# Kernel optimization log

Measured on AMD Instinct MI355X. Metric: run time of the kernel, lower is better.

Reference implementation:

```python
import jax, jax.numpy as jnp
import numpy as np

L, B, T, C, H, V = 12, 4, 1024, 768, 12, 50257
D = C // H
SCALE = 1.0 / float(np.sqrt(D))
EPS = 1e-5


def layernorm(x, g, b):
    m = jnp.mean(x, axis=-1, keepdims=True)
    v = jnp.var(x, axis=-1, keepdims=True)
    return (x - m) / jnp.sqrt(v + EPS) * g + b


def setup_inputs() -> dict:
    key = jax.random.key(0)
    ks = jax.random.split(key, 12)
    w = lambda k, shape: jax.random.normal(k, shape, jnp.float32) * 0.02
    return {
        "idx": jax.random.randint(ks[0], (B, T), 0, V),
        "tok_emb": w(ks[1], (V, C)),
        "pos_emb": w(ks[2], (1, T, C)),
        # per-layer stacked params (leading dim L); Linear stored [in, out]
        "wq": w(ks[3], (L, C, C)), "bq": jnp.zeros((L, C)),
        "wk": w(ks[4], (L, C, C)), "bk": jnp.zeros((L, C)),
        "wv": w(ks[5], (L, C, C)), "bv": jnp.zeros((L, C)),
        "wo": w(ks[6], (L, C, C)), "bo": jnp.zeros((L, C)),
        "ln1_g": jnp.ones((L, C)), "ln1_b": jnp.zeros((L, C)),
        "ln2_g": jnp.ones((L, C)), "ln2_b": jnp.zeros((L, C)),
        "w1": w(ks[7], (L, C, 4 * C)), "b1": jnp.zeros((L, 4 * C)),
        "w2": w(ks[8], (L, 4 * C, C)), "b2": jnp.zeros((L, C)),
        "lnf_g": jnp.ones((C,)), "lnf_b": jnp.zeros((C,)),
        "head_w": w(ks[9], (C, V)),
    }


def gpt_forward(idx, tok_emb, pos_emb, wq, bq, wk, bk, wv, bv, wo, bo,
                ln1_g, ln1_b, ln2_g, ln2_b, w1, b1, w2, b2,
                lnf_g, lnf_b, head_w):
    t = idx.shape[1]
    x = tok_emb[idx] + pos_emb[:, :t, :]                     # [B,T,C]
    mask = jnp.tril(jnp.ones((t, t), dtype=bool))            # causal

    def block(x, p):
        (pwq, pbq, pwk, pbk, pwv, pbv, pwo, pbo,
         g1, be1, g2, be2, pw1, pb1, pw2, pb2) = p
        h = layernorm(x, g1, be1)
        q = (h @ pwq + pbq).reshape(B, t, H, D)
        k = (h @ pwk + pbk).reshape(B, t, H, D)
        v = (h @ pwv + pbv).reshape(B, t, H, D)
        att = jnp.einsum('bthd,bshd->bhts', q, k) * SCALE    # [B,H,T,T]
        att = jnp.where(mask, att, -jnp.inf)
        att = jax.nn.softmax(att, axis=-1)
        y = jnp.einsum('bhts,bshd->bthd', att, v).reshape(B, t, C)
        x = x + y @ pwo + pbo
        h = layernorm(x, g2, be2)
        x = x + jax.nn.gelu(h @ pw1 + pb1, approximate=False) @ pw2 + pb2
        return x, None

    x, _ = jax.lax.scan(block, x, (wq, bq, wk, bk, wv, bv, wo, bo,
                                   ln1_g, ln1_b, ln2_g, ln2_b,
                                   w1, b1, w2, b2))
    x = layernorm(x, lnf_g, lnf_b)
    return x @ head_w                                        # logits [B,T,V]


def reference(idx, tok_emb, pos_emb, wq, bq, wk, bk, wv, bv, wo, bo,
              ln1_g, ln1_b, ln2_g, ln2_b, w1, b1, w2, b2,
              lnf_g, lnf_b, head_w):
    return gpt_forward(idx, tok_emb, pos_emb, wq, bq, wk, bk, wv, bv, wo, bo,
                       ln1_g, ln1_b, ln2_g, ln2_b, w1, b1, w2, b2,
                       lnf_g, lnf_b, head_w)
```

## Files before the change

### kernel.cpp

```cpp
#include <hip/hip_runtime.h>
#include <hip/hip_bf16.h>
#include <math.h>

#define L_ 12
#define B_ 4
#define T_ 1024
#define C_ 768
#define H_ 12
#define D_ 64
#define V_ 50257
#define M_ 4096
#define QKVN 2304
#define FF_ 3072
#define VPAD_ 51200

typedef __hip_bfloat16 bf16;
typedef __attribute__((ext_vector_type(4))) float f32x4;
typedef __attribute__((ext_vector_type(4))) short short4v;
typedef __attribute__((ext_vector_type(8))) short short8;
typedef __attribute__((ext_vector_type(8))) __bf16 bf16x8;

typedef __attribute__((address_space(1))) void gvoid;
typedef __attribute__((address_space(3))) void svoid;

__device__ __forceinline__ f32x4 mfma_bf16(short8 a, short8 b, f32x4 c) {
  return __builtin_amdgcn_mfma_f32_16x16x32_bf16(
      __builtin_bit_cast(bf16x8, a), __builtin_bit_cast(bf16x8, b), c, 0, 0, 0);
}

__device__ __forceinline__ void gload_lds16(const void* g, void* l) {
  __builtin_amdgcn_global_load_lds((gvoid*)(void*)g, (svoid*)l, 16, 0, 0);
}

__device__ __forceinline__ short f2bf(float x) {
  return __builtin_bit_cast(short, __float2bfloat16(x));
}

__global__ __launch_bounds__(256) void embed_kernel(const int* __restrict__ idx,
    const float* __restrict__ tok, const float* __restrict__ pos, float* __restrict__ x)
{
  const int row = blockIdx.x;
  const int t = row & (T_ - 1);
  const int id = idx[row];
  const float* te = tok + (size_t)id * C_;
  const float* pe = pos + (size_t)t * C_;
  float* xr = x + (size_t)row * C_;
  const int tid = threadIdx.x;
  xr[tid]       = te[tid]       + pe[tid];
  xr[tid + 256] = te[tid + 256] + pe[tid + 256];
  xr[tid + 512] = te[tid + 512] + pe[tid + 512];
}

__global__ __launch_bounds__(256) void ln_kernel(const float* __restrict__ x,
    const float* __restrict__ g, const float* __restrict__ be, bf16* __restrict__ out)
{
  const int w = threadIdx.x >> 6, l = threadIdx.x & 63;
  const int row = blockIdx.x * 4 + w;
  const float* xr = x + (size_t)row * C_;
  f32x4 v[3];
  float s = 0.0f, ss = 0.0f;
#pragma unroll
  for (int p = 0; p < 3; p++) {
    v[p] = *(const f32x4*)&xr[p * 256 + l * 4];
#pragma unroll
    for (int e = 0; e < 4; e++) { s += v[p][e]; ss += v[p][e] * v[p][e]; }
  }
#pragma unroll
  for (int o = 32; o >= 1; o >>= 1) { s += __shfl_xor(s, o, 64); ss += __shfl_xor(ss, o, 64); }
  const float mean = s * (1.0f / C_);
  const float rstd = rsqrtf(ss * (1.0f / C_) - mean * mean + 1e-5f);
  bf16* orow = out + (size_t)row * C_;
#pragma unroll
  for (int p = 0; p < 3; p++) {
    const f32x4 gg = *(const f32x4*)&g[p * 256 + l * 4];
    const f32x4 bb = *(const f32x4*)&be[p * 256 + l * 4];
    short4v o4;
#pragma unroll
    for (int e = 0; e < 4; e++) o4[e] = f2bf((v[p][e] - mean) * rstd * gg[e] + bb[e]);
    *(short4v*)&orow[p * 256 + l * 4] = o4;
  }
}

__global__ __launch_bounds__(256) void convt_kernel(const float* __restrict__ in,
    bf16* __restrict__ out, int K, int N, long in_ls, long out_ls, int row_off)
{
  __shared__ float tile[64][65];
  in  += (size_t)blockIdx.z * in_ls;
  out += (size_t)blockIdx.z * out_ls;
  const int k0 = blockIdx.x * 64, n0 = blockIdx.y * 64;
  const int tid = threadIdx.x;
#pragma unroll
  for (int ph = 0; ph < 4; ph++) {
    const int lk = ph * 16 + (tid >> 4);
    const int ln = (tid & 15) * 4;
    const int gn = n0 + ln;
    const float* src = &in[(size_t)(k0 + lk) * N + gn];
    f32x4 vv;
    if (gn + 4 <= N) {
      vv = *(const f32x4*)src;
    } else {
#pragma unroll
      for (int e = 0; e < 4; e++) vv[e] = (gn + e < N) ? src[e] : 0.0f;
    }
    *(f32x4*)&tile[lk][ln] = vv;
  }
  __syncthreads();
#pragma unroll
  for (int ph = 0; ph < 2; ph++) {
    const int lon = ph * 32 + (tid >> 3);
    const int lok0 = (tid & 7) * 8;
    short8 o;
#pragma unroll
    for (int e = 0; e < 8; e++) o[e] = f2bf(tile[lok0 + e][lon]);
    *(short8*)&out[(size_t)(row_off + n0 + lon) * K + k0 + lok0] = o;
  }
}

__global__ __launch_bounds__(256) void packb_kernel(const float* __restrict__ bq,
    const float* __restrict__ bk, const float* __restrict__ bv, float* __restrict__ out)
{
  const int i = blockIdx.x * 256 + threadIdx.x;
  const int ly = i / QKVN, c = i % QKVN;
  float v;
  if (c < C_)            v = bq[ly * C_ + c];
  else if (c < 2 * C_)   v = bk[ly * C_ + c - C_];
  else                   v = bv[ly * C_ + c - 2 * C_];
  out[i] = v;
}

template<bool BIAS, bool GELU, bool RESID, bool BF16OUT, bool VT>
__global__ __launch_bounds__(256) void gemm_bt(
    const short* __restrict__ A, const short* __restrict__ Bt,
    const float* __restrict__ bias, const float* resid,
    void* out, short* __restrict__ vt, int M, int N, int K)
{
  __shared__ short As[128 * 64];
  __shared__ short Bs[128 * 64];
  const int tid = threadIdx.x;
  const int w = tid >> 6, l = tid & 63;
  const int l15 = l & 15, l4 = l >> 4;
  const int wr = w >> 1, wc = w & 1;
  const int nwg = gridDim.x * gridDim.y;
  const int id = blockIdx.y * gridDim.x + blockIdx.x;
  const int chunk = nwg >> 3;
  const int swz = (id & 7) * chunk + (id >> 3);
  const long m0 = (long)(swz % gridDim.x) * 128;
  const long n0 = (long)(swz / gridDim.x) * 128;

  f32x4 acc[4][4] = {};
  const int lrow8 = l >> 3;
  const int lc = l & 7;

  for (int kt = 0; kt < K; kt += 64) {
#pragma unroll
    for (int j = 0; j < 8; j++) {
      const int c = w * 8 + j;
      const int isA = (c < 16);
      const int cc = isA ? c : (c - 16);
      const int row = cc * 8 + lrow8;
      const int colsw = ((lc ^ (row & 7)) << 3);
      const short* gp = (isA ? A + (size_t)(m0 + row) * K : Bt + (size_t)(n0 + row) * K) + kt + colsw;
      short* sp = (isA ? As : Bs) + row * 64 + (lc << 3);
      gload_lds16(gp, sp);
    }
    __syncthreads();
#pragma unroll
    for (int ks = 0; ks < 2; ks++) {
      short8 af[4], bfr[4];
#pragma unroll
      for (int i = 0; i < 4; i++) {
        int row = wr * 64 + i * 16 + l15;
        int cs = (ks * 32 + l4 * 8) ^ ((row & 7) << 3);
        af[i] = *(const short8*)&As[row * 64 + cs];
      }
#pragma unroll
      for (int jn = 0; jn < 4; jn++) {
        int row = wc * 64 + jn * 16 + l15;
        int cs = (ks * 32 + l4 * 8) ^ ((row & 7) << 3);
        bfr[jn] = *(const short8*)&Bs[row * 64 + cs];
      }
#pragma unroll
      for (int i = 0; i < 4; i++)
#pragma unroll
        for (int jn = 0; jn < 4; jn++)
          acc[i][jn] = mfma_bf16(af[i], bfr[jn], acc[i][jn]);
    }
    __syncthreads();
  }

#pragma unroll
  for (int i = 0; i < 4; i++) {
    const long rbase = m0 + wr * 64 + i * 16 + l4 * 4;
#pragma unroll
    for (int jn = 0; jn < 4; jn++) {
      const long col = n0 + wc * 64 + jn * 16 + l15;
      const float bv = BIAS ? bias[col] : 0.0f;
      if (VT && col >= 2 * C_) {
        const int hd = (int)col - 2 * C_;
        const int b = (int)(rbase >> 10);
        const int t0 = (int)(rbase & 1023);
        short4v o4;
#pragma unroll
        for (int r = 0; r < 4; r++) o4[r] = f2bf(acc[i][jn][r] + bv);
        *(short4v*)&vt[((size_t)(b * H_) * D_ + hd) * T_ + t0] = o4;
      } else {
#pragma unroll
        for (int r = 0; r < 4; r++) {
          float v = acc[i][jn][r] + bv;
          if (GELU) v = 0.5f * v * (1.0f + erff(v * 0.70710678118654752f));
          const size_t o = (size_t)(rbase + r) * (size_t)N + col;
          if (RESID)        ((float*)out)[o] = resid[o] + v;
          else if (BF16OUT) ((bf16*)out)[o] = __float2bfloat16(v);
          else              ((float*)out)[o] = v;
        }
      }
    }
  }
}

template<bool BIAS, bool GELU, bool RESID, bool BF16OUT>
__global__ __launch_bounds__(256) void gemm64(
    const short* __restrict__ A, const short* __restrict__ Bt,
    const float* __restrict__ bias, const float* resid,
    void* out, int M, int N, int K)
{
  __shared__ short As[64 * 64];
  __shared__ short Bs[128 * 64];
  const int tid = threadIdx.x;
  const int w = tid >> 6, l = tid & 63;
  const int l15 = l & 15, l4 = l >> 4;
  const int wm = w >> 1, wn = w & 1;
  const int nwg = gridDim.x * gridDim.y;
  const int id = blockIdx.y * gridDim.x + blockIdx.x;
  const int chunk = nwg >> 3;
  const int swz = (id & 7) * chunk + (id >> 3);
  const long m0 = (long)(swz % gridDim.x) * 64;
  const long n0 = (long)(swz / gridDim.x) * 128;
  const int rr = tid >> 3, g = tid & 7;

  f32x4 acc[2][4] = {};

  for (int kt = 0; kt < K; kt += 64) {
#pragma unroll
    for (int p = 0; p < 2; p++) {
      const int row = p * 32 + rr;
      const int cg = ((g ^ (row & 7)) << 3);
      gload_lds16(A + (size_t)(m0 + row) * K + kt + cg, &As[row * 64 + g * 8]);
    }
#pragma unroll
    for (int p = 0; p < 4; p++) {
      const int row = p * 32 + rr;
      const int cg = ((g ^ (row & 7)) << 3);
      gload_lds16(Bt + (size_t)(n0 + row) * K + kt + cg, &Bs[row * 64 + g * 8]);
    }
    __syncthreads();
#pragma unroll
    for (int ks = 0; ks < 2; ks++) {
      short8 af[2], bfr[4];
#pragma unroll
      for (int i = 0; i < 2; i++) {
        int row = wm * 32 + i * 16 + l15;
        int cs = (ks * 32 + l4 * 8) ^ ((row & 7) << 3);
        af[i] = *(const short8*)&As[row * 64 + cs];
      }
#pragma unroll
      for (int j = 0; j < 4; j++) {
        int row = wn * 64 + j * 16 + l15;
        int cs = (ks * 32 + l4 * 8) ^ ((row & 7) << 3);
        bfr[j] = *(const short8*)&Bs[row * 64 + cs];
      }
#pragma unroll
      for (int i = 0; i < 2; i++)
#pragma unroll
        for (int j = 0; j < 4; j++)
          acc[i][j] = mfma_bf16(af[i], bfr[j], acc[i][j]);
    }
    __syncthreads();
  }

#pragma unroll
  for (int i = 0; i < 2; i++) {
    const long rbase = m0 + wm * 32 + i * 16 + l4 * 4;
#pragma unroll
    for (int j = 0; j < 4; j++) {
      const long col = n0 + wn * 64 + j * 16 + l15;
      const float bv = BIAS ? bias[col] : 0.0f;
#pragma unroll
      for (int r = 0; r < 4; r++) {
        float v = acc[i][j][r] + bv;
        if (GELU) v = 0.5f * v * (1.0f + erff(v * 0.70710678118654752f));
        const size_t o = (size_t)(rbase + r) * (size_t)N + col;
        if (RESID)        ((float*)out)[o] = resid[o] + v;
        else if (BF16OUT) ((bf16*)out)[o] = __float2bfloat16(v);
        else              ((float*)out)[o] = v;
      }
    }
  }
}

__global__ __launch_bounds__(512, 1) void gemm256(
    const short* __restrict__ A, const short* __restrict__ Bt,
    float* __restrict__ out, int N, int K)
{
  __shared__ short As[2][256 * 64];
  __shared__ short Bs[2][256 * 64];
  const int tid = threadIdx.x;
  const int l = tid & 63, l15 = l & 15, l4 = l >> 4;
  const int wv = tid >> 6, wm = wv >> 2, wn = wv & 3;
  const int bid = blockIdx.x;
  const int x = bid & 7, r = bid >> 3;
  const int mt = (x & 1) * 8 + (r & 7);
  const int nt = (x >> 1) * 50 + (r >> 3);
  const long m0 = (long)mt * 256;
  const long n0 = (long)nt * 256;
  const int nkt = K >> 6;
  const int rr = tid >> 3, g = tid & 7;

  f32x4 acc[8][4] = {};

  auto stA = [&](int s, int kt, int off) {
#pragma unroll
    for (int p = 0; p < 2; p++) {
      const int row = p * 128 + off + rr;
      gload_lds16(A + (size_t)(m0 + row) * K + (kt << 6) + ((g ^ (row & 7)) << 3),
                  &As[s][row * 64 + g * 8]);
    }
  };
  auto stB = [&](int s, int kt, int off) {
#pragma unroll
    for (int p = 0; p < 2; p++) {
      const int row = p * 128 + ((rr >> 5) << 6) + (rr & 31) + off;
      gload_lds16(Bt + (size_t)(n0 + row) * K + (kt << 6) + ((g ^ (row & 7)) << 3),
                  &Bs[s][row * 64 + g * 8]);
    }
  };
  auto rdA = [&](int s, int mf, int ks) {
    const int row = wm * 128 + mf * 16 + l15;
    const int cs = (ks * 32 + l4 * 8) ^ ((row & 7) << 3);
    return *(const short8*)&As[s][row * 64 + cs];
  };
  auto rdB = [&](int s, int nf, int ks) {
    const int row = wn * 64 + nf * 16 + l15;
    const int cs = (ks * 32 + l4 * 8) ^ ((row & 7) << 3);
    return *(const short8*)&Bs[s][row * 64 + cs];
  };

  stA(0, 0, 0); stB(0, 0, 0); stA(0, 0, 64); stB(0, 0, 32);

  int q = 0;
  for (int kt = 0; kt < nkt; ++kt, q ^= 1) {
    const int ktn = (kt + 1 < nkt) ? kt + 1 : kt;
    short8 a0[2][4], a1[2][4], b0[2][2], b1[2][2];

    stA(q ^ 1, ktn, 0);
    asm volatile("s_waitcnt vmcnt(6)" ::: "memory");
    __builtin_amdgcn_s_barrier();
#pragma unroll
    for (int ks = 0; ks < 2; ks++) {
#pragma unroll
      for (int f = 0; f < 4; f++) a0[ks][f] = rdA(q, f, ks);
#pragma unroll
      for (int j = 0; j < 2; j++) b0[ks][j] = rdB(q, j, ks);
    }
    __builtin_amdgcn_s_setprio(1);
#pragma unroll
    for (int f = 0; f < 4; f++)
#pragma unroll
      for (int j = 0; j < 2; j++) {
        acc[f][j] = mfma_bf16(a0[0][f], b0[0][j], acc[f][j]);
        acc[f][j] = mfma_bf16(a0[1][f], b0[1][j], acc[f][j]);
      }
    __builtin_amdgcn_s_setprio(0);

    stB(q ^ 1, ktn, 0);
    asm volatile("s_waitcnt vmcnt(6)" ::: "memory");
    __builtin_amdgcn_s_barrier();
#pragma unroll
    for (int ks = 0; ks < 2; ks++)
#pragma unroll
      for (int f = 0; f < 4; f++) a1[ks][f] = rdA(q, f + 4, ks);
    __builtin_amdgcn_s_setprio(1);
#pragma unroll
    for (int f = 0; f < 4; f++)
#pragma unroll
      for (int j = 0; j < 2; j++) {
        acc[f + 4][j] = mfma_bf16(a1[0][f], b0[0][j], acc[f + 4][j]);
        acc[f + 4][j] = mfma_bf16(a1[1][f], b0[1][j], acc[f + 4][j]);
      }
    __builtin_amdgcn_s_setprio(0);

    stA(q ^ 1, ktn, 64);
    asm volatile("s_waitcnt vmcnt(6)" ::: "memory");
    __builtin_amdgcn_s_barrier();
#pragma unroll
    for (int ks = 0; ks < 2; ks++)
#pragma unroll
      for (int j = 0; j < 2; j++) b1[ks][j] = rdB(q, j + 2, ks);
    __builtin_amdgcn_s_setprio(1);
#pragma unroll
    for (int f = 0; f < 4; f++)
#pragma unroll
      for (int j = 0; j < 2; j++) {
        acc[f][j + 2] = mfma_bf16(a0[0][f], b1[0][j], acc[f][j + 2]);
        acc[f][j + 2] = mfma_bf16(a0[1][f], b1[1][j], acc[f][j + 2]);
      }
    __builtin_amdgcn_s_setprio(0);

    stB(q ^ 1, ktn, 32);
    __builtin_amdgcn_s_setprio(1);
#pragma unroll
    for (int f = 0; f < 4; f++)
#pragma unroll
      for (int j = 0; j < 2; j++) {
        acc[f + 4][j + 2] = mfma_bf16(a1[0][f], b1[0][j], acc[f + 4][j + 2]);
        acc[f + 4][j + 2] = mfma_bf16(a1[1][f], b1[1][j], acc[f + 4][j + 2]);
      }
    __builtin_amdgcn_s_setprio(0);
  }

#pragma unroll
  for (int i = 0; i < 8; i++) {
#pragma unroll
    for (int j = 0; j < 4; j++) {
      const long col = n0 + wn * 64 + j * 16 + l15;
      if (col >= N) continue;
#pragma unroll
      for (int r2 = 0; r2 < 4; r2++) {
        const long row = m0 + wm * 128 + i * 16 + l4 * 4 + r2;
        out[(size_t)row * (size_t)N + col] = acc[i][j][r2];
      }
    }
  }
}

__global__ __launch_bounds__(256) void attn_kernel(const short* __restrict__ qkv,
    const short* __restrict__ vt, bf16* __restrict__ y)
{
  __shared__ short Ks[2][64 * 64];
  __shared__ short Vs[2][64 * 64];
  const int qt = (gridDim.x - 1) - blockIdx.x;
  const int bh = blockIdx.y;
  const int b = bh / H_, h = bh % H_;
  const int tid = threadIdx.x, w = tid >> 6, l = tid & 63;
  const int l15 = l & 15, l4 = l >> 4;
  const int qrow0 = qt * 64 + w * 16;
  const float SC2 = 0.125f * 1.44269504088896f;

  auto stageKV = [&](int s, int s0) {
    const short* kbase = qkv + (size_t)(b * T_ + s0) * QKVN + C_ + h * D_;
    const short* vsrc = vt + (size_t)bh * D_ * T_ + s0;
#pragma unroll
    for (int ph = 0; ph < 2; ph++) {
      int r = ph * 32 + (tid >> 3);
      int gk = ((tid & 7) ^ ((r & 3) | (((r >> 3) & 1) << 2))) << 3;
      int gv = ((tid & 7) ^ (r & 7)) << 3;
      gload_lds16(kbase + (size_t)r * QKVN + gk, &Ks[s][r * 64 + (tid & 7) * 8]);
      gload_lds16(vsrc + (size_t)r * T_ + gv, &Vs[s][r * 64 + (tid & 7) * 8]);
    }
  };

  short8 qf[2];
#pragma unroll
  for (int kf = 0; kf < 2; kf++)
    qf[kf] = *(const short8*)&qkv[(size_t)(b * T_ + qrow0 + l15) * QKVN + h * D_ + kf * 32 + l4 * 8];

  f32x4 O[4] = {};
  float mst = -1e30f, lst = 0.0f;

  stageKV(0, 0);
  __syncthreads();

  int cur = 0;
  const int qg = qrow0 + l15;
  const int send = qt * 64 + 64;
  for (int s0 = 0; s0 < send; s0 += 64) {
    if (s0 + 64 < send) stageKV(cur ^ 1, s0 + 64);
    f32x4 S[4];
#pragma unroll
    for (int c = 0; c < 4; c++) {
      const int row = 8 * (l15 >> 2) + (l15 & 3) + 4 * (c & 1) + 32 * (c >> 1);
      const int swz = (row & 3) | (((row >> 3) & 1) << 2);
      short8 k0 = *(const short8*)&Ks[cur][row * 64 + ((l4 ^ swz) << 3)];
      short8 k1 = *(const short8*)&Ks[cur][row * 64 + (((4 + l4) ^ swz) << 3)];
      f32x4 z = {0.0f, 0.0f, 0.0f, 0.0f};
      z = mfma_bf16(k0, qf[0], z);
      z = mfma_bf16(k1, qf[1], z);
      S[c] = z;
    }
#pragma unroll
    for (int c = 0; c < 4; c++) {
      const int kvb = s0 + 8 * l4 + 4 * (c & 1) + 32 * (c >> 1);
#pragma unroll
      for (int r = 0; r < 4; r++) {
        const float v = S[c][r] * SC2;
        S[c][r] = (kvb + r <= qg) ? v : -1e30f;
      }
    }
    float pm = -1e30f;
#pragma unroll
    for (int c = 0; c < 4; c++)
#pragma unroll
      for (int r = 0; r < 4; r++) pm = fmaxf(pm, S[c][r]);
    float mn;
    if (__all(pm - mst <= 8.0f)) {
      mn = mst;
    } else {
      float pm2 = fmaxf(pm, __shfl_xor(pm, 16, 64));
      pm2 = fmaxf(pm2, __shfl_xor(pm2, 32, 64));
      mn = fmaxf(mst, pm2);
      const float al = exp2f(mst - mn);
      mst = mn;
      lst *= al;
#pragma unroll
      for (int r = 0; r < 4; r++) {
        const float alr = __shfl(al, l4 * 4 + r, 16);
#pragma unroll
        for (int df = 0; df < 4; df++) O[df][r] *= alr;
      }
    }
    float rs = 0.0f;
    float pvv[4][4];
#pragma unroll
    for (int c = 0; c < 4; c++)
#pragma unroll
      for (int r = 0; r < 4; r++) { pvv[c][r] = exp2f(S[c][r] - mn); rs += pvv[c][r]; }
    rs += __shfl_xor(rs, 16, 64);
    rs += __shfl_xor(rs, 32, 64);
    lst += rs;
    short8 pa[2];
#pragma unroll
    for (int ks = 0; ks < 2; ks++)
#pragma unroll
      for (int r = 0; r < 4; r++) {
        pa[ks][r]     = f2bf(pvv[2 * ks][r]);
        pa[ks][r + 4] = f2bf(pvv[2 * ks + 1][r]);
      }
#pragma unroll
    for (int df = 0; df < 4; df++) {
      const int row = df * 16 + l15;
      short8 v0 = *(const short8*)&Vs[cur][row * 64 + ((l4 ^ (row & 7)) << 3)];
      short8 v1 = *(const short8*)&Vs[cur][row * 64 + ((((4 + l4)) ^ (row & 7)) << 3)];
      O[df] = mfma_bf16(pa[0], v0, O[df]);
      O[df] = mfma_bf16(pa[1], v1, O[df]);
    }
    __syncthreads();
    cur ^= 1;
  }

  const float inv = 1.0f / lst;
#pragma unroll
  for (int r = 0; r < 4; r++) {
    const float invr = __shfl(inv, l4 * 4 + r, 16);
    const size_t row = (size_t)(b * T_ + qrow0 + l4 * 4 + r);
#pragma unroll
    for (int df = 0; df < 4; df++)
      y[row * C_ + h * D_ + df * 16 + l15] = __float2bfloat16(O[df][r] * invr);
  }
}

extern "C" void kernel_launch(void* const* d_in, const int* in_sizes, int n_in,
                              void* d_out, int out_size, void* d_ws, size_t ws_size,
                              hipStream_t stream)
{
  const int*   idx  = (const int*)d_in[0];
  const float* tok  = (const float*)d_in[1];
  const float* pos  = (const float*)d_in[2];
  const float* wq   = (const float*)d_in[3];
  const float* bq   = (const float*)d_in[4];
  const float* wk   = (const float*)d_in[5];
  const float* bk   = (const float*)d_in[6];
  const float* wv   = (const float*)d_in[7];
  const float* bv   = (const float*)d_in[8];
  const float* wo   = (const float*)d_in[9];
  const float* bo   = (const float*)d_in[10];
  const float* ln1g = (const float*)d_in[11];
  const float* ln1b = (const float*)d_in[12];
  const float* ln2g = (const float*)d_in[13];
  const float* ln2b = (const float*)d_in[14];
  const float* w1   = (const float*)d_in[15];
  const float* b1   = (const float*)d_in[16];
  const float* w2   = (const float*)d_in[17];
  const float* b2   = (const float*)d_in[18];
  const float* lnfg = (const float*)d_in[19];
  const float* lnfb = (const float*)d_in[20];
  const float* headw= (const float*)d_in[21];

  char* p = (char*)d_ws;
  size_t off = 0;
  auto alloc = [&](size_t n) { void* r = p + off; off += (n + 255) & ~(size_t)255; return r; };
  short* qkvT  = (short*)alloc((size_t)L_ * QKVN * C_ * 2);
  short* woT   = (short*)alloc((size_t)L_ * C_ * C_ * 2);
  short* w1T   = (short*)alloc((size_t)L_ * FF_ * C_ * 2);
  short* w2T   = (short*)alloc((size_t)L_ * C_ * FF_ * 2);
  short* headT = (short*)alloc((size_t)VPAD_ * C_ * 2);
  float* qkvb  = (float*)alloc((size_t)L_ * QKVN * 4);
  float* x     = (float*)alloc((size_t)M_ * C_ * 4);
  bf16*  h     = (bf16*)alloc((size_t)M_ * C_ * 2);
  short* qkvB  = (short*)alloc((size_t)M_ * QKVN * 2);
  short* vt    = (short*)alloc((size_t)B_ * H_ * D_ * T_ * 2);
  short* y     = (short*)alloc((size_t)M_ * C_ * 2);
  short* hid   = (short*)alloc((size_t)M_ * FF_ * 2);
  if (off > ws_size) return;

  convt_kernel<<<dim3(12, 12, 12), 256, 0, stream>>>(wq, (bf16*)qkvT, C_, C_, (long)C_ * C_, (long)QKVN * C_, 0);
  convt_kernel<<<dim3(12, 12, 12), 256, 0, stream>>>(wk, (bf16*)qkvT, C_, C_, (long)C_ * C_, (long)QKVN * C_, C_);
  convt_kernel<<<dim3(12, 12, 12), 256, 0, stream>>>(wv, (bf16*)qkvT, C_, C_, (long)C_ * C_, (long)QKVN * C_, 2 * C_);
  convt_kernel<<<dim3(12, 12, 12), 256, 0, stream>>>(wo, (bf16*)woT, C_, C_, (long)C_ * C_, (long)C_ * C_, 0);
  convt_kernel<<<dim3(12, 48, 12), 256, 0, stream>>>(w1, (bf16*)w1T, C_, FF_, (long)C_ * FF_, (long)FF_ * C_, 0);
  convt_kernel<<<dim3(48, 12, 12), 256, 0, stream>>>(w2, (bf16*)w2T, FF_, C_, (long)FF_ * C_, (long)C_ * FF_, 0);
  convt_kernel<<<dim3(12, VPAD_ / 64, 1), 256, 0, stream>>>(headw, (bf16*)headT, C_, V_, 0, 0, 0);
  packb_kernel<<<dim3(108), 256, 0, stream>>>(bq, bk, bv, qkvb);

  embed_kernel<<<dim3(M_), 256, 0, stream>>>(idx, tok, pos, x);

  for (int ly = 0; ly < L_; ly++) {
    ln_kernel<<<dim3(M_ / 4), 256, 0, stream>>>(x, ln1g + ly * C_, ln1b + ly * C_, h);
    gemm_bt<true, false, false, true, true><<<dim3(32, 18), 256, 0, stream>>>(
        (const short*)h, qkvT + (size_t)ly * QKVN * C_, qkvb + ly * QKVN, nullptr, qkvB, vt, M_, QKVN, C_);
    attn_kernel<<<dim3(16, 48), 256, 0, stream>>>(qkvB, vt, (bf16*)y);
    gemm64<true, false, true, false><<<dim3(64, 6), 256, 0, stream>>>(
        y, woT + (size_t)ly * C_ * C_, bo + ly * C_, x, x, M_, C_, C_);
    ln_kernel<<<dim3(M_ / 4), 256, 0, stream>>>(x, ln2g + ly * C_, ln2b + ly * C_, h);
    gemm_bt<true, true, false, true, false><<<dim3(32, 24), 256, 0, stream>>>(
        (const short*)h, w1T + (size_t)ly * FF_ * C_, b1 + ly * FF_, nullptr, hid, nullptr, M_, FF_, C_);
    gemm64<true, false, true, false><<<dim3(64, 6), 256, 0, stream>>>(
        hid, w2T + (size_t)ly * C_ * FF_, b2 + ly * C_, x, x, M_, C_, FF_);
  }

  ln_kernel<<<dim3(M_ / 4), 256, 0, stream>>>(x, lnfg, lnfb, h);
  gemm256<<<dim3(3200), 512, 0, stream>>>((const short*)h, headT, (float*)d_out, V_, C_);
}
```

Baseline: 3.040 ms.

## Process 128 query rows per attention block, two 16-row sub-tiles per wave

```diff
diff --git a/kernel.cpp b/kernel.cpp
--- a/kernel.cpp
+++ b/kernel.cpp
@@ -443,7 +443,7 @@
   const int b = bh / H_, h = bh % H_;
   const int tid = threadIdx.x, w = tid >> 6, l = tid & 63;
   const int l15 = l & 15, l4 = l >> 4;
-  const int qrow0 = qt * 64 + w * 16;
+  const int qrow0 = qt * 128 + w * 32;
   const float SC2 = 0.125f * 1.44269504088896f;
 
   auto stageKV = [&](int s, int s0) {
@@ -459,102 +459,116 @@
     }
   };
 
-  short8 qf[2];
-#pragma unroll
-  for (int kf = 0; kf < 2; kf++)
-    qf[kf] = *(const short8*)&qkv[(size_t)(b * T_ + qrow0 + l15) * QKVN + h * D_ + kf * 32 + l4 * 8];
-
-  f32x4 O[4] = {};
-  float mst = -1e30f, lst = 0.0f;
+  short8 qf[2][2];
+#pragma unroll
+  for (int s = 0; s < 2; s++)
+#pragma unroll
+    for (int kf = 0; kf < 2; kf++)
+      qf[s][kf] = *(const short8*)&qkv[(size_t)(b * T_ + qrow0 + s * 16 + l15) * QKVN + h * D_ + kf * 32 + l4 * 8];
+
+  f32x4 O[2][4] = {};
+  float mst[2] = {-1e30f, -1e30f}, lst[2] = {0.0f, 0.0f};
 
   stageKV(0, 0);
   __syncthreads();
 
   int cur = 0;
-  const int qg = qrow0 + l15;
-  const int send = qt * 64 + 64;
+  const int send = qt * 128 + 128;
   for (int s0 = 0; s0 < send; s0 += 64) {
     if (s0 + 64 < send) stageKV(cur ^ 1, s0 + 64);
-    f32x4 S[4];
+    f32x4 S[2][4];
 #pragma unroll
     for (int c = 0; c < 4; c++) {
       const int row = 8 * (l15 >> 2) + (l15 & 3) + 4 * (c & 1) + 32 * (c >> 1);
       const int swz = (row & 3) | (((row >> 3) & 1) << 2);
       short8 k0 = *(const short8*)&Ks[cur][row * 64 + ((l4 ^ swz) << 3)];
       short8 k1 = *(const short8*)&Ks[cur][row * 64 + (((4 + l4) ^ swz) << 3)];
-      f32x4 z = {0.0f, 0.0f, 0.0f, 0.0f};
-      z = mfma_bf16(k0, qf[0], z);
-      z = mfma_bf16(k1, qf[1], z);
-      S[c] = z;
-    }
-#pragma unroll
-    for (int c = 0; c < 4; c++) {
-      const int kvb = s0 + 8 * l4 + 4 * (c & 1) + 32 * (c >> 1);
-#pragma unroll
-      for (int r = 0; r < 4; r++) {
-        const float v = S[c][r] * SC2;
-        S[c][r] = (kvb + r <= qg) ? v : -1e30f;
-      }
-    }
-    float pm = -1e30f;
-#pragma unroll
-    for (int c = 0; c < 4; c++)
-#pragma unroll
-      for (int r = 0; r < 4; r++) pm = fmaxf(pm, S[c][r]);
-    float mn;
-    if (__all(pm - mst <= 8.0f)) {
-      mn = mst;
-    } else {
-      float pm2 = fmaxf(pm, __shfl_xor(pm, 16, 64));
-      pm2 = fmaxf(pm2, __shfl_xor(pm2, 32, 64));
-      mn = fmaxf(mst, pm2);
-      const float al = exp2f(mst - mn);
-      mst = mn;
-      lst *= al;
-#pragma unroll
-      for (int r = 0; r < 4; r++) {
-        const float alr = __shfl(al, l4 * 4 + r, 16);
-#pragma unroll
-        for (int df = 0; df < 4; df++) O[df][r] *= alr;
-      }
-    }
-    float rs = 0.0f;
-    float pvv[4][4];
-#pragma unroll
-    for (int c = 0; c < 4; c++)
-#pragma unroll
-      for (int r = 0; r < 4; r++) { pvv[c][r] = exp2f(S[c][r] - mn); rs += pvv[c][r]; }
-    rs += __shfl_xor(rs, 16, 64);
-    rs += __shfl_xor(rs, 32, 64);
-    lst += rs;
-    short8 pa[2];
-#pragma unroll
-    for (int ks = 0; ks < 2; ks++)
-#pragma unroll
-      for (int r = 0; r < 4; r++) {
-        pa[ks][r]     = f2bf(pvv[2 * ks][r]);
-        pa[ks][r + 4] = f2bf(pvv[2 * ks + 1][r]);
-      }
+#pragma unroll
+      for (int s = 0; s < 2; s++) {
+        f32x4 z = {0.0f, 0.0f, 0.0f, 0.0f};
+        z = mfma_bf16(k0, qf[s][0], z);
+        z = mfma_bf16(k1, qf[s][1], z);
+        S[s][c] = z;
+      }
+    }
+    short8 pa[2][2];
+#pragma unroll
+    for (int s = 0; s < 2; s++) {
+      const int qg = qrow0 + s * 16 + l15;
+#pragma unroll
+      for (int c = 0; c < 4; c++) {
+        const int kvb = s0 + 8 * l4 + 4 * (c & 1) + 32 * (c >> 1);
+#pragma unroll
+        for (int r = 0; r < 4; r++) {
+          const float v = S[s][c][r] * SC2;
+          S[s][c][r] = (kvb + r <= qg) ? v : -1e30f;
+        }
+      }
+      float pm = -1e30f;
+#pragma unroll
+      for (int c = 0; c < 4; c++)
+#pragma unroll
+        for (int r = 0; r < 4; r++) pm = fmaxf(pm, S[s][c][r]);
+      float mn;
+      if (__all(pm - mst[s] <= 8.0f)) {
+        mn = mst[s];
+      } else {
+        float pm2 = fmaxf(pm, __shfl_xor(pm, 16, 64));
+        pm2 = fmaxf(pm2, __shfl_xor(pm2, 32, 64));
+        mn = fmaxf(mst[s], pm2);
+        const float al = exp2f(mst[s] - mn);
+        mst[s] = mn;
+        lst[s] *= al;
+#pragma unroll
+        for (int r = 0; r < 4; r++) {
+          const float alr = __shfl(al, l4 * 4 + r, 16);
+#pragma unroll
+          for (int df = 0; df < 4; df++) O[s][df][r] *= alr;
+        }
+      }
+      float rs = 0.0f;
+      float pvv[4][4];
+#pragma unroll
+      for (int c = 0; c < 4; c++)
+#pragma unroll
+        for (int r = 0; r < 4; r++) { pvv[c][r] = exp2f(S[s][c][r] - mn); rs += pvv[c][r]; }
+      rs += __shfl_xor(rs, 16, 64);
+      rs += __shfl_xor(rs, 32, 64);
+      lst[s] += rs;
+#pragma unroll
+      for (int ks = 0; ks < 2; ks++)
+#pragma unroll
+        for (int r = 0; r < 4; r++) {
+          pa[s][ks][r]     = f2bf(pvv[2 * ks][r]);
+          pa[s][ks][r + 4] = f2bf(pvv[2 * ks + 1][r]);
+        }
+    }
 #pragma unroll
     for (int df = 0; df < 4; df++) {
       const int row = df * 16 + l15;
       short8 v0 = *(const short8*)&Vs[cur][row * 64 + ((l4 ^ (row & 7)) << 3)];
       short8 v1 = *(const short8*)&Vs[cur][row * 64 + ((((4 + l4)) ^ (row & 7)) << 3)];
-      O[df] = mfma_bf16(pa[0], v0, O[df]);
-      O[df] = mfma_bf16(pa[1], v1, O[df]);
+#pragma unroll
+      for (int s = 0; s < 2; s++) {
+        O[s][df] = mfma_bf16(pa[s][0], v0, O[s][df]);
+        O[s][df] = mfma_bf16(pa[s][1], v1, O[s][df]);
+      }
     }
     __syncthreads();
     cur ^= 1;
   }
 
-  const float inv = 1.0f / lst;
-#pragma unroll
-  for (int r = 0; r < 4; r++) {
-    const float invr = __shfl(inv, l4 * 4 + r, 16);
-    const size_t row = (size_t)(b * T_ + qrow0 + l4 * 4 + r);
-#pragma unroll
-    for (int df = 0; df < 4; df++)
-      y[row * C_ + h * D_ + df * 16 + l15] = __float2bfloat16(O[df][r] * invr);
+#pragma unroll
+  for (int s = 0; s < 2; s++) {
+    const float inv = 1.0f / lst[s];
+#pragma unroll
+    for (int r = 0; r < 4; r++) {
+      const float invr = __shfl(inv, l4 * 4 + r, 16);
+      const size_t row = (size_t)(b * T_ + qrow0 + s * 16 + l4 * 4 + r);
+#pragma unroll
+      for (int df = 0; df < 4; df++)
+        y[row * C_ + h * D_ + df * 16 + l15] = __float2bfloat16(O[s][df][r] * invr);
+    }
   }
 }
 
@@ -617,7 +631,7 @@
     ln_kernel<<<dim3(M_ / 4), 256, 0, stream>>>(x, ln1g + ly * C_, ln1b + ly * C_, h);
     gemm_bt<true, false, false, true, true><<<dim3(32, 18), 256, 0, stream>>>(
         (const short*)h, qkvT + (size_t)ly * QKVN * C_, qkvb + ly * QKVN, nullptr, qkvB, vt, M_, QKVN, C_);
-    attn_kernel<<<dim3(16, 48), 256, 0, stream>>>(qkvB, vt, (bf16*)y);
+    attn_kernel<<<dim3(8, 48), 256, 0, stream>>>(qkvB, vt, (bf16*)y);
     gemm64<true, false, true, false><<<dim3(64, 6), 256, 0, stream>>>(
         y, woT + (size_t)ly * C_ * C_, bo + ly * C_, x, x, M_, C_, C_);
     ln_kernel<<<dim3(M_ / 4), 256, 0, stream>>>(x, ln2g + ly * C_, ln2b + ly * C_, h);
```

New measurement: 3.101 ms. +2.0%, slower.
